# Kernel optimization log

Hardware: AMD Instinct MI355X
Metric: run time of the kernel (lower is better)

Reference implementation:

```python
import jax, jax.numpy as jnp
import numpy as np

B, S, D, H, F = 2, 1024, 2048, 16, 8192
DH = D // H
MAX_ALPHA = 0.2
CN_SCALE = D / (D - 1)  # CenterNorm scale factor dim/(dim-1)


def setup_inputs() -> dict:
    key = jax.random.key(0)
    ks = jax.random.split(key, 8)
    s = 0.02
    f32 = jnp.float32
    return {
        "x": jax.random.normal(ks[0], (B, S, D), f32),
        "ln1_g": jnp.ones((D,), f32), "ln1_b": jnp.zeros((D,), f32),
        "wq": jax.random.normal(ks[1], (D, D), f32) * s, "bq": jnp.zeros((D,), f32),
        "wk": jax.random.normal(ks[2], (D, D), f32) * s, "bk": jnp.zeros((D,), f32),
        "wv": jax.random.normal(ks[3], (D, D), f32) * s, "bv": jnp.zeros((D,), f32),
        "wo": jax.random.normal(ks[4], (D, D), f32) * s, "bo": jnp.zeros((D,), f32),
        "tau": jnp.ones((H,), f32),   # learnable per-head temperature, init_tau=1.0
        "nu": jnp.ones((H,), f32),    # learnable per-head output scale, init_nu=1.0
        "alpha1": jnp.full((D,), 0.1, f32),  # per-channel residual weight, init 0.1
        "ln2_g": jnp.ones((D,), f32), "ln2_b": jnp.zeros((D,), f32),
        "w1": jax.random.normal(ks[5], (F, D), f32) * s, "b1": jnp.zeros((F,), f32),
        "w2": jax.random.normal(ks[6], (D, F), f32) * s, "b2": jnp.zeros((D,), f32),
        "alpha2": jnp.full((D,), 0.1, f32),
    }


def _center_norm(x, g, b):
    # CenterNorm: subtract mean only (no variance), scale by dim/(dim-1)
    mu = jnp.mean(x, axis=-1, keepdims=True)
    return g * (CN_SCALE * (x - mu)) + b


def _l2norm(t):
    return t / (jnp.linalg.norm(t, axis=-1, keepdims=True) + 1e-6)


def _cosine_attn(x, wq, bq, wk, bk, wv, bv, wo, bo, tau, nu):
    # project and split heads -> [B,H,S,DH]
    def proj(w, b):
        return (jnp.einsum('bsd,ed->bse', x, w) + b).reshape(B, S, H, DH).transpose(0, 2, 1, 3)
    q, k, v = proj(wq, bq), proj(wk, bk), proj(wv, bv)
    qn, kn = _l2norm(q), _l2norm(k)  # cosine similarity attention
    scores = jnp.einsum('bhqd,bhkd->bhqk', qn, kn) * tau[None, :, None, None]
    causal = jnp.tril(jnp.ones((S, S), bool))
    scores = jnp.where(causal[None, None], scores, -jnp.inf)
    p = jax.nn.softmax(scores, axis=-1)
    o = jnp.einsum('bhqk,bhkd->bhqd', p, v) * nu[None, :, None, None]
    o = o.transpose(0, 2, 1, 3).reshape(B, S, D)
    return jnp.einsum('bsd,ed->bse', o, wo) + bo


def _ffn(x, w1, b1, w2, b2):
    h = jax.nn.gelu(jnp.einsum('bsd,fd->bsf', x, w1) + b1)
    return jnp.einsum('bsf,df->bsd', h, w2) + b2


def reference(x, ln1_g, ln1_b, wq, bq, wk, bk, wv, bv, wo, bo, tau, nu,
              alpha1, ln2_g, ln2_b, w1, b1, w2, b2, alpha2):
    a = _center_norm(x, ln1_g, ln1_b)
    a1 = jnp.clip(alpha1, -MAX_ALPHA, MAX_ALPHA)
    x1 = a + a1 * _cosine_attn(a, wq, bq, wk, bk, wv, bv, wo, bo, tau, nu)
    m = _center_norm(x1, ln2_g, ln2_b)
    a2 = jnp.clip(alpha2, -MAX_ALPHA, MAX_ALPHA)
    return m + a2 * _ffn(m, w1, b1, w2, b2)
```

## Files before the change

kernel.cpp:

```cpp
#include <hip/hip_runtime.h>
#include <hip/hip_bf16.h>
#include <stdint.h>

#define B_ 2
#define S_ 1024
#define D_ 2048
#define H_ 16
#define F_ 8192
#define DH_ 128
#define M_ 2048

typedef unsigned short u16;
typedef __attribute__((ext_vector_type(8))) short short8;
typedef __attribute__((ext_vector_type(4))) float f32x4;
typedef __attribute__((ext_vector_type(2))) float f32x2;
typedef __attribute__((ext_vector_type(2))) unsigned short u16x2;

__device__ __forceinline__ u16 f2bf(float f) {
  union { float f; uint32_t u; } c; c.f = f;
  uint32_t r = c.u + 0x7FFFu + ((c.u >> 16) & 1u);
  return (u16)(r >> 16);
}

__device__ __forceinline__ void gload16(const void* g, void* l) {
  __builtin_amdgcn_global_load_lds((const __attribute__((address_space(1))) void*)g,
                                   (__attribute__((address_space(3))) void*)l, 16, 0, 0);
}

__device__ __forceinline__ float clipa(float a) {
  return fminf(0.2f, fmaxf(-0.2f, a));
}

__device__ __forceinline__ float gelu_f(float x) {
  float z = 0.7978845608028654f * (x + 0.044715f * x * x * x);
  z = fminf(10.f, fmaxf(-10.f, z));
  float e = __expf(2.f * z);
  return 0.5f * x * (1.f + (e - 1.f) / (e + 1.f));
}

__global__ __launch_bounds__(256) void k_cvt(const float* __restrict__ s,
                                             u16* __restrict__ d, int n8) {
  int i = blockIdx.x * 256 + threadIdx.x;
  if (i >= n8) return;
  f32x4 a = *(const f32x4*)(s + (size_t)i * 8);
  f32x4 b = *(const f32x4*)(s + (size_t)i * 8 + 4);
  short8 o;
  o[0] = (short)f2bf(a[0]); o[1] = (short)f2bf(a[1]);
  o[2] = (short)f2bf(a[2]); o[3] = (short)f2bf(a[3]);
  o[4] = (short)f2bf(b[0]); o[5] = (short)f2bf(b[1]);
  o[6] = (short)f2bf(b[2]); o[7] = (short)f2bf(b[3]);
  *(short8*)(d + (size_t)i * 8) = o;
}

__global__ __launch_bounds__(256) void k_centernorm(const float* __restrict__ x,
                                                    const float* __restrict__ g,
                                                    const float* __restrict__ bb,
                                                    float* __restrict__ of,
                                                    u16* __restrict__ ob) {
  const int row = blockIdx.x;
  const int t = threadIdx.x;
  const float* xr = x + (size_t)row * D_;
  f32x4 v0 = *(const f32x4*)(xr + t * 8);
  f32x4 v1 = *(const f32x4*)(xr + t * 8 + 4);
  float s = v0[0] + v0[1] + v0[2] + v0[3] + v1[0] + v1[1] + v1[2] + v1[3];
#pragma unroll
  for (int off = 1; off < 64; off <<= 1) s += __shfl_xor(s, off);
  __shared__ float red[4];
  if ((t & 63) == 0) red[t >> 6] = s;
  __syncthreads();
  const float mu = (red[0] + red[1] + red[2] + red[3]) * (1.0f / D_);
  const float CNS = (float)D_ / (float)(D_ - 1);
  f32x4 g0 = *(const f32x4*)(g + t * 8);
  f32x4 g1 = *(const f32x4*)(g + t * 8 + 4);
  f32x4 b0 = *(const f32x4*)(bb + t * 8);
  f32x4 b1 = *(const f32x4*)(bb + t * 8 + 4);
  f32x4 y0, y1;
  short8 yb;
#pragma unroll
  for (int i = 0; i < 4; i++) {
    y0[i] = g0[i] * (CNS * (v0[i] - mu)) + b0[i];
    y1[i] = g1[i] * (CNS * (v1[i] - mu)) + b1[i];
  }
#pragma unroll
  for (int i = 0; i < 4; i++) { yb[i] = (short)f2bf(y0[i]); yb[4 + i] = (short)f2bf(y1[i]); }
  float* orow = of + (size_t)row * D_;
  *(f32x4*)(orow + t * 8) = y0;
  *(f32x4*)(orow + t * 8 + 4) = y1;
  *(short8*)(ob + (size_t)row * D_ + t * 8) = yb;
}

__global__ __launch_bounds__(256) void k_l2norm(const float* __restrict__ q,
                                                const float* __restrict__ k,
                                                const float* __restrict__ v,
                                                u16* __restrict__ qn,
                                                u16* __restrict__ kn,
                                                u16* __restrict__ vn) {
  const int gw = blockIdx.x * 4 + (threadIdx.x >> 6);
  const int l = threadIdx.x & 63;
  const int h = gw & (H_ - 1);
  const int s = (gw >> 4) & (S_ - 1);
  const int b = gw >> 14;
  const size_t src = ((size_t)(b * S_ + s)) * D_ + h * DH_ + l * 2;
  const size_t dst = (((size_t)(b * H_ + h)) * S_ + s) * DH_ + l * 2;
  {
    f32x2 xv = *(const f32x2*)(q + src);
    float ss = xv[0] * xv[0] + xv[1] * xv[1];
#pragma unroll
    for (int off = 1; off < 64; off <<= 1) ss += __shfl_xor(ss, off);
    float sc = 1.f / (sqrtf(ss) + 1e-6f);
    u16x2 o; o[0] = f2bf(xv[0] * sc); o[1] = f2bf(xv[1] * sc);
    *(u16x2*)(qn + dst) = o;
  }
  {
    f32x2 xv = *(const f32x2*)(k + src);
    float ss = xv[0] * xv[0] + xv[1] * xv[1];
#pragma unroll
    for (int off = 1; off < 64; off <<= 1) ss += __shfl_xor(ss, off);
    float sc = 1.f / (sqrtf(ss) + 1e-6f);
    u16x2 o; o[0] = f2bf(xv[0] * sc); o[1] = f2bf(xv[1] * sc);
    *(u16x2*)(kn + dst) = o;
  }
  {
    f32x2 xv = *(const f32x2*)(v + src);
    u16x2 o; o[0] = f2bf(xv[0]); o[1] = f2bf(xv[1]);
    *(u16x2*)(vn + dst) = o;
  }
}

template <int EPI>
__device__ __forceinline__ void gemm256_core(const u16* __restrict__ A,
                                             const u16* __restrict__ Bt,
                                             const float* __restrict__ bias,
                                             float* __restrict__ outf,
                                             u16* __restrict__ outb,
                                             int N, int K, int kbase, int nk,
                                             int m0, int n0) {
  __shared__ char lds[2][65536];
  const int t = threadIdx.x;
  const int l = t & 63, w = t >> 6;
  const int wr = w >> 2, wc = w & 3;
  const int l15 = l & 15, lhi = l >> 4;
  const int sw = (l15 & 7) << 4;

  auto stage = [&](int region, int half, int kt) {
#pragma unroll
    for (int j = 0; j < 2; j++) {
      const int pl = half * 16384 + j * 8192 + t * 16;
      const int row = pl >> 7;
      const int scol = (pl & 127) ^ ((row & 7) << 4);
      const int grow = (region ? n0 : m0) + row;
      const char* src = (const char*)(region ? Bt : A) +
                        (size_t)grow * (size_t)(K * 2) +
                        (size_t)((kbase + kt * 64) * 2 + scol);
      gload16(src, &lds[kt & 1][region * 32768 + pl]);
    }
  };

  f32x4 acc[8][4] = {};

  stage(1, 0, 0); stage(1, 1, 0); stage(0, 0, 0); stage(0, 1, 0);
  asm volatile("s_waitcnt vmcnt(0)" ::: "memory");
  __builtin_amdgcn_s_barrier();
  __builtin_amdgcn_sched_barrier(0);

  for (int kt = 0; kt < nk; ++kt) {
    const int buf = kt & 1;
    const bool more = (kt + 1 < nk);
    const char* Ab = &lds[buf][0];
    const char* Bb = &lds[buf][32768];
    short8 bf[4][2];
#pragma unroll
    for (int ni = 0; ni < 4; ni++)
#pragma unroll
      for (int ks = 0; ks < 2; ks++) {
        const int r = wc * 64 + ni * 16 + l15;
        bf[ni][ks] = *(const short8*)(Bb + r * 128 + ((ks * 64 + lhi * 16) ^ sw));
      }
#pragma unroll
    for (int q = 0; q < 4; q++) {
      short8 aq[2][2];
#pragma unroll
      for (int mi = 0; mi < 2; mi++)
#pragma unroll
        for (int ks = 0; ks < 2; ks++) {
          const int r = q * 64 + wr * 32 + mi * 16 + l15;
          aq[mi][ks] = *(const short8*)(Ab + r * 128 + ((ks * 64 + lhi * 16) ^ sw));
        }
      if (more) stage(q < 2 ? 1 : 0, q & 1, kt + 1);
      asm volatile("s_waitcnt lgkmcnt(0)" ::: "memory");
      __builtin_amdgcn_sched_barrier(0);
      __builtin_amdgcn_s_setprio(1);
#pragma unroll
      for (int mi = 0; mi < 2; mi++)
#pragma unroll
        for (int ni = 0; ni < 4; ni++)
#pragma unroll
          for (int ks = 0; ks < 2; ks++)
            acc[q * 2 + mi][ni] = __builtin_amdgcn_mfma_f32_16x16x32_bf16(
                aq[mi][ks], bf[ni][ks], acc[q * 2 + mi][ni], 0, 0, 0);
      __builtin_amdgcn_s_setprio(0);
      if (q == 1) {
        if (more) { asm volatile("s_waitcnt vmcnt(4)" ::: "memory"); }
        else      { asm volatile("s_waitcnt vmcnt(0)" ::: "memory"); }
        __builtin_amdgcn_s_barrier();
        __builtin_amdgcn_sched_barrier(0);
      }
      if (q == 3) {
        asm volatile("s_waitcnt vmcnt(2)" ::: "memory");
        __builtin_amdgcn_s_barrier();
        __builtin_amdgcn_sched_barrier(0);
      }
    }
  }

#pragma unroll
  for (int ni = 0; ni < 4; ni++) {
    const int col = n0 + wc * 64 + ni * 16 + l15;
    const float bcol = (EPI == 3) ? 0.f : bias[col];
#pragma unroll
    for (int ai = 0; ai < 8; ai++) {
      const int row = m0 + (ai >> 1) * 64 + wr * 32 + (ai & 1) * 16 + lhi * 4;
#pragma unroll
      for (int j = 0; j < 4; j++) {
        const float v = acc[ai][ni][j] + bcol;
        const size_t idx = (size_t)(row + j) * N + col;
        if (EPI == 0) outf[idx] = v;
        else if (EPI == 2) outb[idx] = f2bf(gelu_f(v));
        else outf[idx] = v;
      }
    }
  }
}

__device__ __forceinline__ void xcd_swz(int gx, int gy, int& bx, int& by) {
  const int nwg = gx * gy;
  const int bid = blockIdx.y * gx + blockIdx.x;
  const int s = (bid & 7) * (nwg >> 3) + (bid >> 3);
  bx = s % gx;
  by = s / gx;
}

__global__ __launch_bounds__(512, 2) void k_qkv256(const u16* A, const u16* W,
                                                   const float* b0, const float* b1,
                                                   const float* b2, float* o0, float* o1,
                                                   float* o2) {
  const int z = blockIdx.z;
  const u16* Bt = W + (size_t)z * 4194304;
  const float* bias = z == 0 ? b0 : (z == 1 ? b1 : b2);
  float* out = z == 0 ? o0 : (z == 1 ? o1 : o2);
  int bx, by; xcd_swz(8, 8, bx, by);
  gemm256_core<0>(A, Bt, bias, out, nullptr, D_, D_, 0, 32, by * 256, bx * 256);
}

__global__ __launch_bounds__(512, 2) void k_ffn1_256(const u16* A, const u16* Bt,
                                                     const float* bias, u16* outb) {
  int bx, by; xcd_swz(32, 8, bx, by);
  gemm256_core<2>(A, Bt, bias, nullptr, outb, F_, D_, 0, 32, by * 256, bx * 256);
}

__global__ __launch_bounds__(512, 2) void k_ffn2_256(const u16* A, const u16* Bt, float* P) {
  int bx, by; xcd_swz(8, 8, bx, by);
  gemm256_core<3>(A, Bt, nullptr, P + (size_t)blockIdx.z * M_ * D_, nullptr, D_, F_,
                  blockIdx.z * 2048, 32, by * 256, bx * 256);
}

__device__ __forceinline__ void gemm128_res(const u16* __restrict__ A,
                                            const u16* __restrict__ Bt,
                                            const float* __restrict__ bias,
                                            const float* __restrict__ res,
                                            const float* __restrict__ alpha,
                                            float* __restrict__ outf, int N, int K) {
  __shared__ u16 As[2][128 * 32];
  __shared__ u16 Bs[2][128 * 32];
  const int t = threadIdx.x;
  const int l = t & 63;
  const int w = t >> 6;
  const int wr = w >> 1, wc = w & 1;
  const int l15 = l & 15, lhi = l >> 4;
  const int m0 = blockIdx.y * 128, n0 = blockIdx.x * 128;
  f32x4 acc[4][4] = {};
  const int srow = t >> 2;
  const int scol = (t & 3) * 8;
  const u16* Ag = A + (size_t)(m0 + srow) * K + scol;
  const u16* Ag2 = Ag + (size_t)64 * K;
  const u16* Bg = Bt + (size_t)(n0 + srow) * K + scol;
  const u16* Bg2 = Bg + (size_t)64 * K;
  const int loff = t * 16;
  const int kiters = K / 32;

  gload16(Ag, (char*)As[0] + loff);
  gload16(Ag2, (char*)As[0] + 4096 + loff);
  gload16(Bg, (char*)Bs[0] + loff);
  gload16(Bg2, (char*)Bs[0] + 4096 + loff);
  __syncthreads();

  int cur = 0;
  for (int it = 0; it < kiters; ++it) {
    if (it + 1 < kiters) {
      const int k0 = (it + 1) * 32;
      char* dA = (char*)As[cur ^ 1] + loff;
      char* dB = (char*)Bs[cur ^ 1] + loff;
      gload16(Ag + k0, dA);
      gload16(Ag2 + k0, dA + 4096);
      gload16(Bg + k0, dB);
      gload16(Bg2 + k0, dB + 4096);
    }
    short8 af[4], bfr[4];
#pragma unroll
    for (int i = 0; i < 4; i++)
      af[i] = *(const short8*)(As[cur] + (wr * 64 + i * 16 + l15) * 32 + lhi * 8);
#pragma unroll
    for (int i = 0; i < 4; i++)
      bfr[i] = *(const short8*)(Bs[cur] + (wc * 64 + i * 16 + l15) * 32 + lhi * 8);
#pragma unroll
    for (int mi = 0; mi < 4; mi++)
#pragma unroll
      for (int ni = 0; ni < 4; ni++)
        acc[mi][ni] = __builtin_amdgcn_mfma_f32_16x16x32_bf16(af[mi], bfr[ni], acc[mi][ni], 0, 0, 0);
    __syncthreads();
    cur ^= 1;
  }
#pragma unroll
  for (int ni = 0; ni < 4; ni++) {
    const int col = n0 + wc * 64 + ni * 16 + l15;
    const float bcol = bias[col];
    const float alc = clipa(alpha[col]);
#pragma unroll
    for (int mi = 0; mi < 4; mi++) {
#pragma unroll
      for (int j = 0; j < 4; j++) {
        const int row = m0 + wr * 64 + mi * 16 + lhi * 4 + j;
        const size_t idx = (size_t)row * N + col;
        outf[idx] = res[idx] + alc * (acc[mi][ni][j] + bcol);
      }
    }
  }
}

__global__ __launch_bounds__(256) void k_oproj(const u16* A, const u16* Bt, const float* bias,
                                               const float* res, const float* alpha,
                                               float* outf) {
  gemm128_res(A, Bt, bias, res, alpha, outf, D_, D_);
}

__global__ __launch_bounds__(256) void k_ffn2_combine(const float* __restrict__ P,
                                                      const float* __restrict__ bias,
                                                      const float* __restrict__ res,
                                                      const float* __restrict__ alpha,
                                                      float* __restrict__ out) {
  const int i = blockIdx.x * 256 + threadIdx.x;
  const size_t base = (size_t)i * 8;
  const int col = (int)(base & (D_ - 1));
  const size_t PS = (size_t)M_ * D_;
  f32x4 s0 = {}, s1 = {};
#pragma unroll
  for (int p = 0; p < 4; p++) {
    s0 += *(const f32x4*)(P + p * PS + base);
    s1 += *(const f32x4*)(P + p * PS + base + 4);
  }
  f32x4 b0 = *(const f32x4*)(bias + col);
  f32x4 b1 = *(const f32x4*)(bias + col + 4);
  f32x4 a0 = *(const f32x4*)(alpha + col);
  f32x4 a1 = *(const f32x4*)(alpha + col + 4);
  f32x4 r0 = *(const f32x4*)(res + base);
  f32x4 r1 = *(const f32x4*)(res + base + 4);
  f32x4 o0, o1;
#pragma unroll
  for (int j = 0; j < 4; j++) {
    o0[j] = r0[j] + clipa(a0[j]) * (s0[j] + b0[j]);
    o1[j] = r1[j] + clipa(a1[j]) * (s1[j] + b1[j]);
  }
  *(f32x4*)(out + base) = o0;
  *(f32x4*)(out + base + 4) = o1;
}

__global__ __launch_bounds__(256) void k_attn(const u16* __restrict__ qn,
                                              const u16* __restrict__ kn,
                                              const u16* __restrict__ vn,
                                              const float* __restrict__ tau,
                                              const float* __restrict__ nu,
                                              u16* __restrict__ o) {
  __shared__ u16 Ks[64 * 128];
  __shared__ u16 Vt[128 * 64];
  __shared__ u16 Pl[4][16][72];
  const int t = threadIdx.x;
  const int l = t & 63, w = t >> 6;
  const int l15 = l & 15, lhi = l >> 4;
  const int qt = blockIdx.x;
  const int bh = blockIdx.y;
  const int h = bh & (H_ - 1);
  const int b = bh >> 4;
  const size_t hoff = (size_t)bh * S_ * DH_;
  const u16* Qh = qn + hoff;
  const u16* Kh = kn + hoff;
  const u16* Vh = vn + hoff;
  const int q0 = qt * 64;
  const int r0 = q0 + w * 16;
  short8 qf[4];
#pragma unroll
  for (int kk = 0; kk < 4; kk++)
    qf[kk] = *(const short8*)(Qh + (size_t)(r0 + l15) * DH_ + kk * 32 + lhi * 8);
  const float taum = tau[h];
  float mrow[4], lrow[4];
  f32x4 oacc[8] = {};
#pragma unroll
  for (int j = 0; j < 4; j++) { mrow[j] = -1e30f; lrow[j] = 0.f; }

  for (int kv0 = 0; kv0 < q0 + 64; kv0 += 64) {
#pragma unroll
    for (int i = 0; i < 4; i++) {
      const int p = i * 4096 + t * 16;
      const int row = p >> 8;
      const int colb = p & 255;
      const int scolb = colb ^ ((row & 7) << 4);
      gload16((const char*)(Kh + (size_t)(kv0 + row) * DH_) + scolb, (char*)Ks + p);
    }
#pragma unroll
    for (int i = 0; i < 4; i++) {
      const int c0 = w * 8 + i * 32;
      const int r = l;
      short8 vv = *(const short8*)(Vh + (size_t)(kv0 + r) * DH_ + c0);
#pragma unroll
      for (int j = 0; j < 8; j++) {
        const int ba = ((c0 + j) * 128 + r * 2) ^ (((c0 + j) & 7) << 4);
        *(u16*)((char*)Vt + ba) = (u16)vv[j];
      }
    }
    __syncthreads();
    f32x4 st[4] = {};
#pragma unroll
    for (int ks = 0; ks < 4; ks++) {
#pragma unroll
      for (int ct = 0; ct < 4; ct++) {
        const int n = ct * 16 + l15;
        const int ka = (ks * 32 + lhi * 8) * 2;
        short8 kf = *(const short8*)((const char*)Ks + n * 256 + (ka ^ ((n & 7) << 4)));
        st[ct] = __builtin_amdgcn_mfma_f32_16x16x32_bf16(qf[ks], kf, st[ct], 0, 0, 0);
      }
    }
    float pm[4] = {-1e30f, -1e30f, -1e30f, -1e30f};
#pragma unroll
    for (int ct = 0; ct < 4; ct++) {
      const int col = kv0 + ct * 16 + l15;
#pragma unroll
      for (int j = 0; j < 4; j++) {
        const int row = r0 + lhi * 4 + j;
        float s = st[ct][j] * taum;
        s = (col <= row) ? s : -1e30f;
        st[ct][j] = s;
        pm[j] = fmaxf(pm[j], s);
      }
    }
#pragma unroll
    for (int j = 0; j < 4; j++) {
#pragma unroll
      for (int off = 1; off < 16; off <<= 1) pm[j] = fmaxf(pm[j], __shfl_xor(pm[j], off));
    }
    float scl[4], psum[4];
#pragma unroll
    for (int j = 0; j < 4; j++) {
      const float nm = fmaxf(mrow[j], pm[j]);
      scl[j] = __expf(mrow[j] - nm);
      mrow[j] = nm;
      psum[j] = 0.f;
    }
#pragma unroll
    for (int ct = 0; ct < 4; ct++) {
#pragma unroll
      for (int j = 0; j < 4; j++) {
        const float p = __expf(st[ct][j] - mrow[j]);
        psum[j] += p;
        Pl[w][lhi * 4 + j][ct * 16 + l15] = f2bf(p);
      }
    }
#pragma unroll
    for (int j = 0; j < 4; j++) {
#pragma unroll
      for (int off = 1; off < 16; off <<= 1) psum[j] += __shfl_xor(psum[j], off);
      lrow[j] = lrow[j] * scl[j] + psum[j];
    }
#pragma unroll
    for (int nt = 0; nt < 8; nt++) {
#pragma unroll
      for (int j = 0; j < 4; j++) oacc[nt][j] *= scl[j];
    }
#pragma unroll
    for (int ks2 = 0; ks2 < 2; ks2++) {
      short8 pa = *(const short8*)((const char*)&Pl[w][0][0] + l15 * 144 + ks2 * 64 + lhi * 16);
#pragma unroll
      for (int nt = 0; nt < 8; nt++) {
        const int n = nt * 16 + l15;
        const int ba = (n * 128 + (ks2 * 32 + lhi * 8) * 2) ^ ((n & 7) << 4);
        short8 vf = *(const short8*)((const char*)Vt + ba);
        oacc[nt] = __builtin_amdgcn_mfma_f32_16x16x32_bf16(pa, vf, oacc[nt], 0, 0, 0);
      }
    }
    __syncthreads();
  }
  const float num = nu[h];
  float rs[4];
#pragma unroll
  for (int j = 0; j < 4; j++) rs[j] = num / lrow[j];
#pragma unroll
  for (int nt = 0; nt < 8; nt++) {
    const int col = h * DH_ + nt * 16 + l15;
#pragma unroll
    for (int j = 0; j < 4; j++) {
      const int row = r0 + lhi * 4 + j;
      o[((size_t)b * S_ + row) * D_ + col] = f2bf(oacc[nt][j] * rs[j]);
    }
  }
}

extern "C" void kernel_launch(void* const* d_in, const int* in_sizes, int n_in,
                              void* d_out, int out_size, void* d_ws, size_t ws_size,
                              hipStream_t stream) {
  const float* x    = (const float*)d_in[0];
  const float* ln1g = (const float*)d_in[1];
  const float* ln1b = (const float*)d_in[2];
  const float* wq   = (const float*)d_in[3];
  const float* bq   = (const float*)d_in[4];
  const float* wk   = (const float*)d_in[5];
  const float* bk   = (const float*)d_in[6];
  const float* wv   = (const float*)d_in[7];
  const float* bv   = (const float*)d_in[8];
  const float* wo   = (const float*)d_in[9];
  const float* bo   = (const float*)d_in[10];
  const float* tau  = (const float*)d_in[11];
  const float* nu   = (const float*)d_in[12];
  const float* al1  = (const float*)d_in[13];
  const float* ln2g = (const float*)d_in[14];
  const float* ln2b = (const float*)d_in[15];
  const float* w1   = (const float*)d_in[16];
  const float* b1   = (const float*)d_in[17];
  const float* w2   = (const float*)d_in[18];
  const float* b2   = (const float*)d_in[19];
  const float* al2  = (const float*)d_in[20];

  char* ws = (char*)d_ws;
  u16* WQ = (u16*)(ws + 0);
  u16* WK = (u16*)(ws + 8388608);
  u16* WV = (u16*)(ws + 16777216);
  u16* WO = (u16*)(ws + 25165824);
  u16* W1B = (u16*)(ws + 33554432);
  u16* W2B = (u16*)(ws + 67108864);
  float* AF = (float*)(ws + 100663296);
  u16*   AB = (u16*)(ws + 117440512);
  float* QF = (float*)(ws + 125829120);
  float* KF = (float*)(ws + 142606336);
  float* VF = (float*)(ws + 159383552);
  u16* QN = (u16*)(ws + 176160768);
  u16* KN = (u16*)(ws + 184549376);
  u16* VN = (u16*)(ws + 192937984);
  u16*   OB = (u16*)(ws + 125829120);
  u16*   MB = (u16*)(ws + 134217728);
  float* X1 = (float*)(ws + 142606336);
  float* MF2 = (float*)(ws + 159383552);
  u16*   HB = (u16*)(ws + 176160768);
  float* P4 = (float*)(ws + 0);

  k_cvt<<<2048, 256, 0, stream>>>(wq, WQ, 524288);
  k_cvt<<<2048, 256, 0, stream>>>(wk, WK, 524288);
  k_cvt<<<2048, 256, 0, stream>>>(wv, WV, 524288);
  k_cvt<<<2048, 256, 0, stream>>>(wo, WO, 524288);
  k_cvt<<<8192, 256, 0, stream>>>(w1, W1B, 2097152);
  k_cvt<<<8192, 256, 0, stream>>>(w2, W2B, 2097152);

  k_centernorm<<<M_, 256, 0, stream>>>(x, ln1g, ln1b, AF, AB);

  k_qkv256<<<dim3(8, 8, 3), 512, 0, stream>>>(AB, WQ, bq, bk, bv, QF, KF, VF);

  k_l2norm<<<8192, 256, 0, stream>>>(QF, KF, VF, QN, KN, VN);

  k_attn<<<dim3(S_ / 64, B_ * H_), 256, 0, stream>>>(QN, KN, VN, tau, nu, OB);

  k_oproj<<<dim3(16, 16), 256, 0, stream>>>(OB, WO, bo, AF, al1, X1);

  k_centernorm<<<M_, 256, 0, stream>>>(X1, ln2g, ln2b, MF2, MB);

  k_ffn1_256<<<dim3(32, 8), 512, 0, stream>>>(MB, W1B, b1, HB);

  k_ffn2_256<<<dim3(8, 8, 4), 512, 0, stream>>>(HB, W2B, P4);
  k_ffn2_combine<<<2048, 256, 0, stream>>>(P4, b2, MF2, al2, (float*)d_out);
}
```

Before: 415.0 us.

## Restructure GEMM prefetch to two-stage-ahead with fewer barriers, merge weight conversions

```diff
diff --git a/kernel.cpp b/kernel.cpp
--- a/kernel.cpp
+++ b/kernel.cpp
@@ -38,18 +38,33 @@
   return 0.5f * x * (1.f + (e - 1.f) / (e + 1.f));
 }
 
-__global__ __launch_bounds__(256) void k_cvt(const float* __restrict__ s,
-                                             u16* __restrict__ d, int n8) {
-  int i = blockIdx.x * 256 + threadIdx.x;
-  if (i >= n8) return;
-  f32x4 a = *(const f32x4*)(s + (size_t)i * 8);
-  f32x4 b = *(const f32x4*)(s + (size_t)i * 8 + 4);
+__global__ __launch_bounds__(256) void k_cvt_all(const float* __restrict__ wq,
+                                                 const float* __restrict__ wk,
+                                                 const float* __restrict__ wv,
+                                                 const float* __restrict__ wo,
+                                                 const float* __restrict__ w1,
+                                                 const float* __restrict__ w2,
+                                                 u16* __restrict__ dst) {
+  const int gi = blockIdx.x * 256 + threadIdx.x;
+  const float* s;
+  int off;
+  if (gi < 2097152) {
+    int r = gi >> 19;
+    s = r == 0 ? wq : (r == 1 ? wk : (r == 2 ? wv : wo));
+    off = gi & 524287;
+  } else if (gi < 4194304) {
+    s = w1; off = gi - 2097152;
+  } else {
+    s = w2; off = gi - 4194304;
+  }
+  f32x4 a = *(const f32x4*)(s + (size_t)off * 8);
+  f32x4 b = *(const f32x4*)(s + (size_t)off * 8 + 4);
   short8 o;
   o[0] = (short)f2bf(a[0]); o[1] = (short)f2bf(a[1]);
   o[2] = (short)f2bf(a[2]); o[3] = (short)f2bf(a[3]);
   o[4] = (short)f2bf(b[0]); o[5] = (short)f2bf(b[1]);
   o[6] = (short)f2bf(b[2]); o[7] = (short)f2bf(b[3]);
-  *(short8*)(d + (size_t)i * 8) = o;
+  *(short8*)(dst + (size_t)gi * 8) = o;
 }
 
 __global__ __launch_bounds__(256) void k_centernorm(const float* __restrict__ x,
@@ -141,11 +156,14 @@
   const int wr = w >> 2, wc = w & 3;
   const int l15 = l & 15, lhi = l >> 4;
   const int sw = (l15 & 7) << 4;
-
-  auto stage = [&](int region, int half, int kt) {
-#pragma unroll
-    for (int j = 0; j < 2; j++) {
-      const int pl = half * 16384 + j * 8192 + t * 16;
+  const int ab0 = l15 * 128 + ((lhi * 16) ^ sw);
+  const int ab1 = l15 * 128 + ((64 + lhi * 16) ^ sw);
+
+  auto stage = [&](int kt, int h) {
+#pragma unroll
+    for (int rj = 0; rj < 4; rj++) {
+      const int region = rj >> 1, j = rj & 1;
+      const int pl = h * 16384 + j * 8192 + t * 16;
       const int row = pl >> 7;
       const int scol = (pl & 127) ^ ((row & 7) << 4);
       const int grow = (region ? n0 : m0) + row;
@@ -158,58 +176,50 @@
 
   f32x4 acc[8][4] = {};
 
-  stage(1, 0, 0); stage(1, 1, 0); stage(0, 0, 0); stage(0, 1, 0);
-  asm volatile("s_waitcnt vmcnt(0)" ::: "memory");
+  stage(0, 0); stage(0, 1); stage(1, 0);
+  asm volatile("s_waitcnt vmcnt(4)" ::: "memory");
   __builtin_amdgcn_s_barrier();
   __builtin_amdgcn_sched_barrier(0);
 
   for (int kt = 0; kt < nk; ++kt) {
-    const int buf = kt & 1;
-    const bool more = (kt + 1 < nk);
-    const char* Ab = &lds[buf][0];
-    const char* Bb = &lds[buf][32768];
+    const char* base = &lds[kt & 1][0];
+    const char* pA0 = base + wr * 4096 + ab0;
+    const char* pA1 = base + wr * 4096 + ab1;
+    const char* pB0 = base + 32768 + wc * 8192 + ab0;
+    const char* pB1 = base + 32768 + wc * 8192 + ab1;
     short8 bf[4][2];
 #pragma unroll
-    for (int ni = 0; ni < 4; ni++)
-#pragma unroll
-      for (int ks = 0; ks < 2; ks++) {
-        const int r = wc * 64 + ni * 16 + l15;
-        bf[ni][ks] = *(const short8*)(Bb + r * 128 + ((ks * 64 + lhi * 16) ^ sw));
-      }
+    for (int ni = 0; ni < 4; ni++) {
+      bf[ni][0] = *(const short8*)(pB0 + ni * 2048);
+      bf[ni][1] = *(const short8*)(pB1 + ni * 2048);
+    }
 #pragma unroll
     for (int q = 0; q < 4; q++) {
       short8 aq[2][2];
 #pragma unroll
-      for (int mi = 0; mi < 2; mi++)
-#pragma unroll
-        for (int ks = 0; ks < 2; ks++) {
-          const int r = q * 64 + wr * 32 + mi * 16 + l15;
-          aq[mi][ks] = *(const short8*)(Ab + r * 128 + ((ks * 64 + lhi * 16) ^ sw));
-        }
-      if (more) stage(q < 2 ? 1 : 0, q & 1, kt + 1);
-      asm volatile("s_waitcnt lgkmcnt(0)" ::: "memory");
-      __builtin_amdgcn_sched_barrier(0);
+      for (int mi = 0; mi < 2; mi++) {
+        aq[mi][0] = *(const short8*)(pA0 + q * 8192 + mi * 2048);
+        aq[mi][1] = *(const short8*)(pA1 + q * 8192 + mi * 2048);
+      }
+      if (q == 1 && kt + 1 < nk) stage(kt + 1, 1);
+      if (q == 3 && kt + 2 < nk) stage(kt + 2, 0);
       __builtin_amdgcn_s_setprio(1);
 #pragma unroll
-      for (int mi = 0; mi < 2; mi++)
-#pragma unroll
-        for (int ni = 0; ni < 4; ni++)
-#pragma unroll
-          for (int ks = 0; ks < 2; ks++)
+      for (int ks = 0; ks < 2; ks++)
+#pragma unroll
+        for (int mi = 0; mi < 2; mi++)
+#pragma unroll
+          for (int ni = 0; ni < 4; ni++)
             acc[q * 2 + mi][ni] = __builtin_amdgcn_mfma_f32_16x16x32_bf16(
                 aq[mi][ks], bf[ni][ks], acc[q * 2 + mi][ni], 0, 0, 0);
       __builtin_amdgcn_s_setprio(0);
-      if (q == 1) {
-        if (more) { asm volatile("s_waitcnt vmcnt(4)" ::: "memory"); }
-        else      { asm volatile("s_waitcnt vmcnt(0)" ::: "memory"); }
-        __builtin_amdgcn_s_barrier();
-        __builtin_amdgcn_sched_barrier(0);
-      }
-      if (q == 3) {
-        asm volatile("s_waitcnt vmcnt(2)" ::: "memory");
-        __builtin_amdgcn_s_barrier();
-        __builtin_amdgcn_sched_barrier(0);
-      }
+      if (q == 1) __builtin_amdgcn_s_barrier();
+    }
+    if (kt + 1 < nk) {
+      if (kt + 2 < nk) { asm volatile("s_waitcnt vmcnt(4)" ::: "memory"); }
+      else             { asm volatile("s_waitcnt vmcnt(0)" ::: "memory"); }
+      __builtin_amdgcn_s_barrier();
+      __builtin_amdgcn_sched_barrier(0);
     }
   }
 
@@ -230,14 +240,6 @@
       }
     }
   }
-}
-
-__device__ __forceinline__ void xcd_swz(int gx, int gy, int& bx, int& by) {
-  const int nwg = gx * gy;
-  const int bid = blockIdx.y * gx + blockIdx.x;
-  const int s = (bid & 7) * (nwg >> 3) + (bid >> 3);
-  bx = s % gx;
-  by = s / gx;
 }
 
 __global__ __launch_bounds__(512, 2) void k_qkv256(const u16* A, const u16* W,
@@ -248,20 +250,19 @@
   const u16* Bt = W + (size_t)z * 4194304;
   const float* bias = z == 0 ? b0 : (z == 1 ? b1 : b2);
   float* out = z == 0 ? o0 : (z == 1 ? o1 : o2);
-  int bx, by; xcd_swz(8, 8, bx, by);
-  gemm256_core<0>(A, Bt, bias, out, nullptr, D_, D_, 0, 32, by * 256, bx * 256);
+  gemm256_core<0>(A, Bt, bias, out, nullptr, D_, D_, 0, 32,
+                  blockIdx.y * 256, blockIdx.x * 256);
 }
 
 __global__ __launch_bounds__(512, 2) void k_ffn1_256(const u16* A, const u16* Bt,
                                                      const float* bias, u16* outb) {
-  int bx, by; xcd_swz(32, 8, bx, by);
-  gemm256_core<2>(A, Bt, bias, nullptr, outb, F_, D_, 0, 32, by * 256, bx * 256);
+  gemm256_core<2>(A, Bt, bias, nullptr, outb, F_, D_, 0, 32,
+                  blockIdx.y * 256, blockIdx.x * 256);
 }
 
 __global__ __launch_bounds__(512, 2) void k_ffn2_256(const u16* A, const u16* Bt, float* P) {
-  int bx, by; xcd_swz(8, 8, bx, by);
   gemm256_core<3>(A, Bt, nullptr, P + (size_t)blockIdx.z * M_ * D_, nullptr, D_, F_,
-                  blockIdx.z * 2048, 32, by * 256, bx * 256);
+                  blockIdx.z * 2048, 32, blockIdx.y * 256, blockIdx.x * 256);
 }
 
 __device__ __forceinline__ void gemm128_res(const u16* __restrict__ A,
@@ -539,8 +540,6 @@
 
   char* ws = (char*)d_ws;
   u16* WQ = (u16*)(ws + 0);
-  u16* WK = (u16*)(ws + 8388608);
-  u16* WV = (u16*)(ws + 16777216);
   u16* WO = (u16*)(ws + 25165824);
   u16* W1B = (u16*)(ws + 33554432);
   u16* W2B = (u16*)(ws + 67108864);
@@ -559,12 +558,7 @@
   u16*   HB = (u16*)(ws + 176160768);
   float* P4 = (float*)(ws + 0);
 
-  k_cvt<<<2048, 256, 0, stream>>>(wq, WQ, 524288);
-  k_cvt<<<2048, 256, 0, stream>>>(wk, WK, 524288);
-  k_cvt<<<2048, 256, 0, stream>>>(wv, WV, 524288);
-  k_cvt<<<2048, 256, 0, stream>>>(wo, WO, 524288);
-  k_cvt<<<8192, 256, 0, stream>>>(w1, W1B, 2097152);
-  k_cvt<<<8192, 256, 0, stream>>>(w2, W2B, 2097152);
+  k_cvt_all<<<24576, 256, 0, stream>>>(wq, wk, wv, wo, w1, w2, WQ);
 
   k_centernorm<<<M_, 256, 0, stream>>>(x, ln1g, ln1b, AF, AB);
 
```

Measured after the change: 399.7 us. 1.04x faster.
